# Kernel tuning notes

Hardware: AMD Instinct MI355X
Metric: run time of the kernel (lower is better)

Reference implementation:

```python
import jax, jax.numpy as jnp
import numpy as np

B, T, S, DM, H, HID = 4, 1024, 1024, 1024, 16, 4096
DEPTH = DM // H


def setup_inputs() -> dict:
    key = jax.random.key(0)
    ks = jax.random.split(key, 32)
    n = lambda k, shape, scale=1.0: jax.random.normal(k, shape, dtype=jnp.float32) * scale
    w_scale = 1.0 / np.sqrt(DM)
    inp = {
        "x": n(ks[0], (B, T, DM)),
        "enc_out": n(ks[1], (B, S, DM)),
        # causal mask: 1 where attention is forbidden (TF convention mask*-1e9)
        "look_ahead_mask": jnp.broadcast_to(
            jnp.triu(jnp.ones((T, T), jnp.float32), k=1), (B, 1, T, T)),
        "padding_mask": jnp.zeros((B, 1, 1, S), jnp.float32),
    }
    # self-attention MHA params
    names = ["wq1", "wk1", "wv1", "wo1", "wq2", "wk2", "wv2", "wo2"]
    for i, nm in enumerate(names):
        inp[nm] = n(ks[2 + i], (DM, DM), w_scale)
        inp["b" + nm[1:]] = jnp.zeros((DM,), jnp.float32)
    # FFN
    inp["wh"] = n(ks[10], (DM, HID), w_scale)
    inp["bh"] = jnp.zeros((HID,), jnp.float32)
    inp["wout"] = n(ks[11], (HID, DM), 1.0 / np.sqrt(HID))
    inp["bout"] = jnp.zeros((DM,), jnp.float32)
    for i in (1, 2, 3):
        inp[f"g{i}"] = jnp.ones((DM,), jnp.float32)
        inp[f"be{i}"] = jnp.zeros((DM,), jnp.float32)
    return inp


def _layer_norm(x, gamma, beta, eps=1e-6):
    mean = jnp.mean(x, axis=-1, keepdims=True)
    var = jnp.mean(jnp.square(x - mean), axis=-1, keepdims=True)
    return gamma * (x - mean) * jax.lax.rsqrt(var + eps) + beta


def _mha(q_in, k_in, v_in, mask, wq, bq, wk, bk, wv, bv, wo, bo):
    b = q_in.shape[0]
    split = lambda t: t.reshape(b, -1, H, DEPTH).transpose(0, 2, 1, 3)  # [b,h,s,d]
    Q = split(q_in @ wq + bq)
    K = split(k_in @ wk + bk)
    V = split(v_in @ wv + bv)
    scores = jnp.einsum("bhqd,bhkd->bhqk", Q, K) / jnp.sqrt(jnp.float32(DEPTH))
    scores = scores + mask * (-1e9)
    w = jax.nn.softmax(scores, axis=-1)
    out = jnp.einsum("bhqk,bhkd->bhqd", w, V)
    out = out.transpose(0, 2, 1, 3).reshape(b, -1, DM)
    return out @ wo + bo


def reference(x, enc_out, look_ahead_mask, padding_mask,
              wq1, bq1, wk1, bk1, wv1, bv1, wo1, bo1,
              wq2, bq2, wk2, bk2, wv2, bv2, wo2, bo2,
              wh, bh, wout, bout, g1, be1, g2, be2, g3, be3):
    # self-attention + residual + LN (dropout identity at inference)
    a1 = _mha(x, x, x, look_ahead_mask, wq1, bq1, wk1, bk1, wv1, bv1, wo1, bo1)
    h1 = _layer_norm(a1 + x, g1, be1)
    # cross-attention + residual + LN
    a2 = _mha(h1, enc_out, enc_out, padding_mask,
              wq2, bq2, wk2, bk2, wv2, bv2, wo2, bo2)
    h2 = _layer_norm(a2 + h1, g2, be2)
    # FFN + residual + LN
    f = jax.nn.relu(h2 @ wh + bh) @ wout + bout
    return _layer_norm(f + h2, g3, be3)
```

## Files before the change

kernel.cpp:

```cpp
#include <hip/hip_runtime.h>
#include <hip/hip_bf16.h>

typedef __bf16 bf16;
typedef __bf16 bf16x4 __attribute__((ext_vector_type(4)));
typedef __bf16 bf16x8 __attribute__((ext_vector_type(8)));
typedef float floatx4 __attribute__((ext_vector_type(4)));

#define MFMA16(a, b, c) __builtin_amdgcn_mfma_f32_16x16x32_bf16(a, b, c, 0, 0, 0)

#define BB   4
#define TT   1024
#define SS   1024
#define DMOD 1024
#define NH   16
#define DH   64
#define HID  4096
#define MTOT (BB * TT)

__device__ __forceinline__ float loadf(const bf16* p)  { return (float)*p; }
__device__ __forceinline__ float loadf(const float* p) { return *p; }

__device__ __forceinline__ void gll16(const bf16* g, bf16* l) {
    __builtin_amdgcn_global_load_lds(
        (const __attribute__((address_space(1))) void*)g,
        (__attribute__((address_space(3))) void*)l, 16, 0, 0);
}

struct TBatch { const float* src[8]; bf16* dst[8]; };

__global__ __launch_bounds__(256)
void transpose_sq_kernel(TBatch tb)
{
    __shared__ float t[64][65];
    const float* W = tb.src[blockIdx.z];
    bf16* WT = tb.dst[blockIdx.z];
    const int k0 = blockIdx.y * 64, n0 = blockIdx.x * 64;
    const int tid = threadIdx.x;
    const int r = tid >> 4, c = (tid & 15) * 4;
    #pragma unroll
    for (int i = 0; i < 4; ++i) {
        float4 v = *(const float4*)(W + (size_t)(k0 + i * 16 + r) * DMOD + n0 + c);
        t[i * 16 + r][c + 0] = v.x; t[i * 16 + r][c + 1] = v.y;
        t[i * 16 + r][c + 2] = v.z; t[i * 16 + r][c + 3] = v.w;
    }
    __syncthreads();
    #pragma unroll
    for (int i = 0; i < 4; ++i) {
        int n = i * 16 + r;
        bf16x4 o;
        #pragma unroll
        for (int j = 0; j < 4; ++j) o[j] = (bf16)t[c + j][n];
        *(bf16x4*)(WT + (size_t)(n0 + n) * DMOD + k0 + c) = o;
    }
}

__global__ __launch_bounds__(256)
void transpose_kernel(const float* __restrict__ W, bf16* __restrict__ WT, int K, int N)
{
    __shared__ float t[64][65];
    const int k0 = blockIdx.y * 64, n0 = blockIdx.x * 64;
    const int tid = threadIdx.x;
    const int r = tid >> 4, c = (tid & 15) * 4;
    #pragma unroll
    for (int i = 0; i < 4; ++i) {
        float4 v = *(const float4*)(W + (size_t)(k0 + i * 16 + r) * N + n0 + c);
        t[i * 16 + r][c + 0] = v.x; t[i * 16 + r][c + 1] = v.y;
        t[i * 16 + r][c + 2] = v.z; t[i * 16 + r][c + 3] = v.w;
    }
    __syncthreads();
    #pragma unroll
    for (int i = 0; i < 4; ++i) {
        int n = i * 16 + r;
        bf16x4 o;
        #pragma unroll
        for (int j = 0; j < 4; ++j) o[j] = (bf16)t[c + j][n];
        *(bf16x4*)(WT + (size_t)(n0 + n) * K + k0 + c) = o;
    }
}

__global__ __launch_bounds__(256)
void vtrans_kernel(const bf16* __restrict__ in, int ldi, bf16* __restrict__ out)
{
    __shared__ bf16 t[64][72];
    const int r0 = blockIdx.y * 64;
    const int c0 = blockIdx.x * 64;
    const int tid = threadIdx.x;
    const int rr = tid >> 3;
    const int c8 = (tid & 7) * 8;
    #pragma unroll
    for (int i = 0; i < 2; ++i) {
        int row = i * 32 + rr;
        bf16x8 v = *(const bf16x8*)(in + (size_t)(r0 + row) * ldi + c0 + c8);
        *(bf16x8*)(&t[row][c8]) = v;
    }
    __syncthreads();
    #pragma unroll
    for (int i = 0; i < 2; ++i) {
        int col = i * 32 + rr;
        bf16x8 v;
        #pragma unroll
        for (int j = 0; j < 8; ++j) v[j] = t[c8 + j][col];
        *(bf16x8*)(out + (size_t)(c0 + col) * MTOT + r0 + c8) = v;
    }
}

__global__ __launch_bounds__(256)
void cvt_kernel(const float* __restrict__ in, bf16* __restrict__ out, int n4)
{
    int i = blockIdx.x * 256 + threadIdx.x;
    if (i < n4) {
        float4 v = ((const float4*)in)[i];
        bf16x4 o = { (bf16)v.x, (bf16)v.y, (bf16)v.z, (bf16)v.w };
        ((bf16x4*)out)[i] = o;
    }
}

__global__ __launch_bounds__(256)
void bias_concat_kernel(const float* bq1, const float* bk1, const float* bv1,
                        const float* bk2, const float* bv2, float* __restrict__ biasc)
{
    int i = blockIdx.x * 256 + threadIdx.x;
    float v;
    if      (i < 1024) v = bq1[i];
    else if (i < 2048) v = bk1[i - 1024];
    else if (i < 3072) v = bv1[i - 2048];
    else if (i < 4096) v = bk2[i - 3072];
    else               v = bv2[i - 4096];
    if (i < 5120) biasc[i] = v;
}

template <int EPI, typename TR>
__global__ __launch_bounds__(256, 2)
void gemm_kernel(const bf16* __restrict__ A, int lda, const bf16* __restrict__ B,
                 const float* __restrict__ bias, const TR* __restrict__ resid,
                 bf16* __restrict__ out, int M, int N, int K)
{
    __shared__ bf16 Al[128 * 64];
    __shared__ bf16 Bl[128 * 64];

    const int tid  = threadIdx.x;
    const int wave = tid >> 6;
    const int lane = tid & 63;
    const int l16  = lane & 15;
    const int quad = lane >> 4;
    const int bm   = blockIdx.y * 128;
    const int bn   = blockIdx.x * 128;
    const int wm   = (wave >> 1) * 64;
    const int wn   = (wave & 1) * 64;
    const int lrow = lane >> 3;
    const int lcol = (lane & 7) * 8;

    floatx4 acc[4][4] = {};

    for (int k0 = 0; k0 < K; k0 += 64) {
        __syncthreads();
        #pragma unroll
        for (int t = 0; t < 4; ++t) {
            int r0 = (wave * 4 + t) * 8;
            gll16(A + (size_t)(bm + r0 + lrow) * lda + k0 + lcol, Al + r0 * 64);
            gll16(B + (size_t)(bn + r0 + lrow) * K   + k0 + lcol, Bl + r0 * 64);
        }
        __syncthreads();

        #pragma unroll
        for (int ks = 0; ks < 2; ++ks) {
            bf16x8 af[4], bg[4];
            #pragma unroll
            for (int mt = 0; mt < 4; ++mt)
                af[mt] = *(const bf16x8*)(Al + (wm + mt * 16 + l16) * 64 + ks * 32 + quad * 8);
            #pragma unroll
            for (int nt = 0; nt < 4; ++nt)
                bg[nt] = *(const bf16x8*)(Bl + (wn + nt * 16 + l16) * 64 + ks * 32 + quad * 8);
            #pragma unroll
            for (int mt = 0; mt < 4; ++mt)
                #pragma unroll
                for (int nt = 0; nt < 4; ++nt)
                    acc[mt][nt] = MFMA16(af[mt], bg[nt], acc[mt][nt]);
        }
    }

    #pragma unroll
    for (int mt = 0; mt < 4; ++mt) {
        int row0 = bm + wm + mt * 16 + quad * 4;
        #pragma unroll
        for (int nt = 0; nt < 4; ++nt) {
            int col = bn + wn + nt * 16 + l16;
            float bv = bias[col];
            #pragma unroll
            for (int r = 0; r < 4; ++r) {
                float v = acc[mt][nt][r] + bv;
                size_t idx = (size_t)(row0 + r) * N + col;
                if (EPI == 1) v = fmaxf(v, 0.0f);
                if (EPI == 2) v += loadf(resid + idx);
                out[idx] = (bf16)v;
            }
        }
    }
}

template <int EPI, typename TR>
__global__ __launch_bounds__(256, 2)
void gemm64_kernel(const bf16* __restrict__ A, int lda, const bf16* __restrict__ B,
                   const float* __restrict__ bias, const TR* __restrict__ resid,
                   bf16* __restrict__ out, int M, int N, int K)
{
    __shared__ bf16 Al[64 * 64];
    __shared__ bf16 Bl[128 * 64];

    const int tid  = threadIdx.x;
    const int wave = tid >> 6;
    const int lane = tid & 63;
    const int l16  = lane & 15;
    const int quad = lane >> 4;
    const int bm   = blockIdx.y * 64;
    const int bn   = blockIdx.x * 128;
    const int wm   = (wave >> 1) * 32;
    const int wn   = (wave & 1) * 64;
    const int lrow = lane >> 3;
    const int lcol = (lane & 7) * 8;

    floatx4 acc[2][4] = {};

    for (int k0 = 0; k0 < K; k0 += 64) {
        __syncthreads();
        #pragma unroll
        for (int t = 0; t < 2; ++t) {
            int r0 = wave * 16 + t * 8;
            gll16(A + (size_t)(bm + r0 + lrow) * lda + k0 + lcol, Al + r0 * 64);
        }
        #pragma unroll
        for (int t = 0; t < 4; ++t) {
            int r0 = (wave * 4 + t) * 8;
            gll16(B + (size_t)(bn + r0 + lrow) * K + k0 + lcol, Bl + r0 * 64);
        }
        __syncthreads();

        #pragma unroll
        for (int ks = 0; ks < 2; ++ks) {
            bf16x8 af[2], bg[4];
            #pragma unroll
            for (int mt = 0; mt < 2; ++mt)
                af[mt] = *(const bf16x8*)(Al + (wm + mt * 16 + l16) * 64 + ks * 32 + quad * 8);
            #pragma unroll
            for (int nt = 0; nt < 4; ++nt)
                bg[nt] = *(const bf16x8*)(Bl + (wn + nt * 16 + l16) * 64 + ks * 32 + quad * 8);
            #pragma unroll
            for (int mt = 0; mt < 2; ++mt)
                #pragma unroll
                for (int nt = 0; nt < 4; ++nt)
                    acc[mt][nt] = MFMA16(af[mt], bg[nt], acc[mt][nt]);
        }
    }

    #pragma unroll
    for (int mt = 0; mt < 2; ++mt) {
        int row0 = bm + wm + mt * 16 + quad * 4;
        #pragma unroll
        for (int nt = 0; nt < 4; ++nt) {
            int col = bn + wn + nt * 16 + l16;
            float bv = bias[col];
            #pragma unroll
            for (int r = 0; r < 4; ++r) {
                float v = acc[mt][nt][r] + bv;
                size_t idx = (size_t)(row0 + r) * N + col;
                if (EPI == 1) v = fmaxf(v, 0.0f);
                if (EPI == 2) v += loadf(resid + idx);
                out[idx] = (bf16)v;
            }
        }
    }
}

template <int CAUSAL>
__global__ __launch_bounds__(256, 2)
void attn_kernel(const bf16* __restrict__ Q, int ldq, const bf16* __restrict__ K, int ldk,
                 const bf16* __restrict__ Vt, bf16* __restrict__ O, int ldo)
{
    __shared__ bf16 Kl[64 * 64];
    __shared__ bf16 Vl[64 * 64];
    __shared__ bf16 Pl[4 * 16 * 72];

    const int tid  = threadIdx.x;
    const int wave = tid >> 6;
    const int lane = tid & 63;
    const int l16  = lane & 15;
    const int quad = lane >> 4;
    const int qb   = CAUSAL ? (15 - blockIdx.x) : blockIdx.x;
    const int h    = blockIdx.y;
    const int b    = blockIdx.z;

    const int qrow0 = b * TT + qb * 64 + wave * 16;
    const int colh  = h * DH;
    const int lr8   = lane >> 3;
    const int lc8   = (lane & 7) * 8;

    bf16x8 qa[2];
    #pragma unroll
    for (int c = 0; c < 2; ++c)
        qa[c] = *(const bf16x8*)(Q + (size_t)(qrow0 + l16) * ldq + colh + c * 32 + quad * 8);

    floatx4 o[5] = {};
    const float C = 0.125f * 1.4426950408889634f;
    bf16x8 onesf;
    {
        bf16 ov = (bf16)((l16 == 0) ? 1.0f : 0.0f);
        #pragma unroll
        for (int j = 0; j < 8; ++j) onesf[j] = ov;
    }

    const int ntiles = CAUSAL ? qb + 1 : (SS / 64);
    bf16* pw = Pl + wave * (16 * 72);

    for (int t = 0; t < ntiles; ++t) {
        const int kv0 = t * 64;
        __syncthreads();
        #pragma unroll
        for (int i = 0; i < 2; ++i) {
            int r0 = wave * 16 + i * 8;
            gll16(K  + (size_t)(b * SS + kv0 + r0 + lr8) * ldk + colh + lc8, Kl + r0 * 64);
            gll16(Vt + (size_t)(colh + r0 + lr8) * MTOT + b * SS + kv0 + lc8, Vl + r0 * 64);
        }
        __syncthreads();

        floatx4 s[4];
        #pragma unroll
        for (int nt = 0; nt < 4; ++nt) {
            bf16x8 kb0 = *(const bf16x8*)(Kl + (nt * 16 + l16) * 64 + quad * 8);
            bf16x8 kb1 = *(const bf16x8*)(Kl + (nt * 16 + l16) * 64 + 32 + quad * 8);
            floatx4 z = {};
            z = MFMA16(qa[0], kb0, z);
            z = MFMA16(qa[1], kb1, z);
            s[nt] = z;
        }

        const bool dm = CAUSAL && (t == qb);
        #pragma unroll
        for (int nt = 0; nt < 4; ++nt)
            #pragma unroll
            for (int r = 0; r < 4; ++r) {
                float sv = s[nt][r] * C;
                if (dm) {
                    int qg  = wave * 16 + quad * 4 + r;
                    int kvg = nt * 16 + l16;
                    if (kvg > qg) sv = -1e30f;
                }
                float pv = exp2f(sv);
                pw[(quad * 4 + r) * 72 + nt * 16 + l16] = (bf16)pv;
            }

        bf16x8 pa0 = *(const bf16x8*)(pw + l16 * 72 + quad * 8);
        bf16x8 pa1 = *(const bf16x8*)(pw + l16 * 72 + 32 + quad * 8);
        #pragma unroll
        for (int dt = 0; dt < 4; ++dt) {
            bf16x8 vb0 = *(const bf16x8*)(Vl + (dt * 16 + l16) * 64 + quad * 8);
            bf16x8 vb1 = *(const bf16x8*)(Vl + (dt * 16 + l16) * 64 + 32 + quad * 8);
            o[dt] = MFMA16(pa0, vb0, o[dt]);
            o[dt] = MFMA16(pa1, vb1, o[dt]);
        }
        o[4] = MFMA16(pa0, onesf, o[4]);
        o[4] = MFMA16(pa1, onesf, o[4]);
    }

    #pragma unroll
    for (int r = 0; r < 4; ++r) {
        float lr  = __shfl(o[4][r], (lane & 48));
        float inv = __builtin_amdgcn_rcpf(lr);
        #pragma unroll
        for (int dt = 0; dt < 4; ++dt) {
            float ov = o[dt][r] * inv;
            size_t idx = (size_t)(qrow0 + quad * 4 + r) * ldo + colh + dt * 16 + l16;
            O[idx] = (bf16)ov;
        }
    }
}

template <typename TO>
__global__ __launch_bounds__(256)
void ln_kernel(const bf16* __restrict__ in, const float* __restrict__ g,
               const float* __restrict__ be, TO* __restrict__ out)
{
    const int row = blockIdx.x;
    const int tid = threadIdx.x;
    bf16x4 xv = *(const bf16x4*)(in + (size_t)row * DMOD + tid * 4);
    float x0 = (float)xv[0], x1 = (float)xv[1], x2 = (float)xv[2], x3 = (float)xv[3];

    float s = x0 + x1 + x2 + x3;
    #pragma unroll
    for (int off = 32; off >= 1; off >>= 1) s += __shfl_xor(s, off);
    __shared__ float red1[4];
    __shared__ float red2[4];
    const int wave = tid >> 6;
    if ((tid & 63) == 0) red1[wave] = s;
    __syncthreads();
    float mean = (red1[0] + red1[1] + red1[2] + red1[3]) * (1.0f / DMOD);

    float d0 = x0 - mean, d1 = x1 - mean, d2 = x2 - mean, d3 = x3 - mean;
    float sq = d0 * d0 + d1 * d1 + d2 * d2 + d3 * d3;
    #pragma unroll
    for (int off = 32; off >= 1; off >>= 1) sq += __shfl_xor(sq, off);
    if ((tid & 63) == 0) red2[wave] = sq;
    __syncthreads();
    float var = (red2[0] + red2[1] + red2[2] + red2[3]) * (1.0f / DMOD);
    float rs = rsqrtf(var + 1e-6f);

    int c = tid * 4;
    size_t o0 = (size_t)row * DMOD + c;
    out[o0 + 0] = (TO)(g[c + 0] * d0 * rs + be[c + 0]);
    out[o0 + 1] = (TO)(g[c + 1] * d1 * rs + be[c + 1]);
    out[o0 + 2] = (TO)(g[c + 2] * d2 * rs + be[c + 2]);
    out[o0 + 3] = (TO)(g[c + 3] * d3 * rs + be[c + 3]);
}

extern "C" void kernel_launch(void* const* d_in, const int* in_sizes, int n_in,
                              void* d_out, int out_size, void* d_ws, size_t ws_size,
                              hipStream_t stream)
{
    const float* x   = (const float*)d_in[0];
    const float* enc = (const float*)d_in[1];
    const float* wq1 = (const float*)d_in[4];  const float* bq1 = (const float*)d_in[5];
    const float* wk1 = (const float*)d_in[6];  const float* bk1 = (const float*)d_in[7];
    const float* wv1 = (const float*)d_in[8];  const float* bv1 = (const float*)d_in[9];
    const float* wo1 = (const float*)d_in[10]; const float* bo1 = (const float*)d_in[11];
    const float* wq2 = (const float*)d_in[12]; const float* bq2 = (const float*)d_in[13];
    const float* wk2 = (const float*)d_in[14]; const float* bk2 = (const float*)d_in[15];
    const float* wv2 = (const float*)d_in[16]; const float* bv2 = (const float*)d_in[17];
    const float* wo2 = (const float*)d_in[18]; const float* bo2 = (const float*)d_in[19];
    const float* wh  = (const float*)d_in[20]; const float* bh  = (const float*)d_in[21];
    const float* wou = (const float*)d_in[22]; const float* bou = (const float*)d_in[23];
    const float* g1  = (const float*)d_in[24]; const float* be1 = (const float*)d_in[25];
    const float* g2  = (const float*)d_in[26]; const float* be2 = (const float*)d_in[27];
    const float* g3  = (const float*)d_in[28]; const float* be3 = (const float*)d_in[29];

    const int M = MTOT;
    const size_t MB = 1u << 20;
    dim3 blk(256);

    char* ws = (char*)d_ws;
    bf16*  WT    = (bf16*)(ws);
    float* biasc = (float*)(ws + 8 * MB);
    bf16*  xb    = (bf16*)(ws + 9 * MB);
    bf16*  h1    = (bf16*)(ws + 9 * MB);
    bf16*  tmpb3 = (bf16*)(ws + 9 * MB);
    bf16*  encb  = (bf16*)(ws + 17 * MB);
    bf16*  Vt2   = (bf16*)(ws + 17 * MB);
    bf16*  ffn   = (bf16*)(ws + 17 * MB);
    bf16*  qkv   = (bf16*)(ws + 25 * MB);
    bf16*  kvb   = qkv + (size_t)M * 1024;
    bf16*  tmpb2 = qkv + (size_t)M * 1024;
    bf16*  Vt1   = (bf16*)(ws + 49 * MB);
    bf16*  tmpb1 = (bf16*)(ws + 49 * MB);
    bf16*  h2    = (bf16*)(ws + 49 * MB);

    dim3 gThi(HID / 64, DMOD / 64);
    dim3 gTout(DMOD / 64, HID / 64);
    dim3 gVt(DMOD / 64, M / 64);
    dim3 gQKV(3072 / 128, M / 128);
    dim3 gKV(2048 / 128, M / 128);
    dim3 gN64(DMOD / 128, M / 64);
    dim3 gH(HID / 128, M / 128);
    dim3 gA(TT / 64, NH, BB);
    const size_t W1M = (size_t)1024 * 1024;

    cvt_kernel<<<dim3(M * DMOD / 4 / 256), blk, 0, stream>>>(x, xb, M * DMOD / 4);
    cvt_kernel<<<dim3(M * DMOD / 4 / 256), blk, 0, stream>>>(enc, encb, M * DMOD / 4);
    bias_concat_kernel<<<dim3(20), blk, 0, stream>>>(bq1, bk1, bv1, bk2, bv2, biasc);

    {
        TBatch tb;
        tb.src[0] = wq1; tb.dst[0] = WT + 0 * W1M;
        tb.src[1] = wk1; tb.dst[1] = WT + 1 * W1M;
        tb.src[2] = wv1; tb.dst[2] = WT + 2 * W1M;
        tb.src[3] = wo1; tb.dst[3] = WT + 3 * W1M;
        tb.src[4] = tb.src[5] = tb.src[6] = tb.src[7] = wq1;
        tb.dst[4] = tb.dst[5] = tb.dst[6] = tb.dst[7] = WT;
        dim3 g4(16, 16, 4);
        transpose_sq_kernel<<<g4, blk, 0, stream>>>(tb);
    }

    gemm_kernel<0, bf16><<<gQKV, blk, 0, stream>>>(xb, 1024, WT, biasc, (const bf16*)nullptr,
                                                   qkv, M, 3072, 1024);
    vtrans_kernel<<<gVt, blk, 0, stream>>>(qkv + 2048, 3072, Vt1);
    attn_kernel<1><<<gA, blk, 0, stream>>>(qkv, 3072, qkv + 1024, 3072, Vt1, qkv, 3072);
    gemm64_kernel<2, float><<<gN64, blk, 0, stream>>>(qkv, 3072, WT + 3 * W1M, bo1, x,
                                                      tmpb1, M, 1024, 1024);
    ln_kernel<bf16><<<dim3(M), blk, 0, stream>>>(tmpb1, g1, be1, h1);

    {
        TBatch tb;
        tb.src[0] = wq2; tb.dst[0] = WT + 0 * W1M;
        tb.src[1] = wk2; tb.dst[1] = WT + 1 * W1M;
        tb.src[2] = wv2; tb.dst[2] = WT + 2 * W1M;
        tb.src[3] = wo2; tb.dst[3] = WT + 3 * W1M;
        tb.src[4] = tb.src[5] = tb.src[6] = tb.src[7] = wq2;
        tb.dst[4] = tb.dst[5] = tb.dst[6] = tb.dst[7] = WT;
        dim3 g4(16, 16, 4);
        transpose_sq_kernel<<<g4, blk, 0, stream>>>(tb);
    }

    gemm64_kernel<0, bf16><<<gN64, blk, 0, stream>>>(h1, 1024, WT, bq2, (const bf16*)nullptr,
                                                     qkv, M, 1024, 1024);
    gemm_kernel<0, bf16><<<gKV, blk, 0, stream>>>(encb, 1024, WT + 1 * W1M, biasc + 3072,
                                                  (const bf16*)nullptr, kvb, M, 2048, 1024);
    vtrans_kernel<<<gVt, blk, 0, stream>>>(kvb + 1024, 2048, Vt2);
    attn_kernel<0><<<gA, blk, 0, stream>>>(qkv, 1024, kvb, 2048, Vt2, qkv, 1024);
    gemm64_kernel<2, bf16><<<gN64, blk, 0, stream>>>(qkv, 1024, WT + 3 * W1M, bo2, h1,
                                                     tmpb2, M, 1024, 1024);
    ln_kernel<bf16><<<dim3(M), blk, 0, stream>>>(tmpb2, g2, be2, h2);

    transpose_kernel<<<gThi, blk, 0, stream>>>(wh, WT, DMOD, HID);
    gemm_kernel<1, bf16><<<gH, blk, 0, stream>>>(h2, 1024, WT, bh, (const bf16*)nullptr,
                                                 ffn, M, HID, 1024);
    transpose_kernel<<<gTout, blk, 0, stream>>>(wou, WT, HID, DMOD);
    gemm64_kernel<2, bf16><<<gN64, blk, 0, stream>>>(ffn, 4096, WT, bou, h2,
                                                     tmpb3, M, 1024, 4096);
    ln_kernel<float><<<dim3(M), blk, 0, stream>>>(tmpb3, g3, be3, (float*)d_out);
}
```

Baseline: 573.4 us.

## Double-buffer LDS tiles with prefetch and XOR-swizzle in GEMM and attention

Converts the GEMM, GEMM64 and attention kernels to double-buffered LDS: each loop iteration issues global-to-LDS loads for the next K or KV tile before running MFMAs on the current one, and uses a single barrier per iteration instead of two. It also XOR-swizzles the 16-byte column chunks within each 64-element row, both when staging and when reading fragments, to reduce LDS bank conflicts. LDS use doubles (64KB for the 128x128 GEMM), which may limit the two-blocks-per-CU occupancy target.

Measured after the change: 543.6 us. 1.05x faster.

```diff
diff --git a/kernel.cpp b/kernel.cpp
--- a/kernel.cpp
+++ b/kernel.cpp
@@ -135,8 +135,8 @@
                  const float* __restrict__ bias, const TR* __restrict__ resid,
                  bf16* __restrict__ out, int M, int N, int K)
 {
-    __shared__ bf16 Al[128 * 64];
-    __shared__ bf16 Bl[128 * 64];
+    __shared__ bf16 Al[2][128 * 64];
+    __shared__ bf16 Bl[2][128 * 64];
 
     const int tid  = threadIdx.x;
     const int wave = tid >> 6;
@@ -148,36 +148,53 @@
     const int wm   = (wave >> 1) * 64;
     const int wn   = (wave & 1) * 64;
     const int lrow = lane >> 3;
-    const int lcol = (lane & 7) * 8;
+    const int scol = ((lane & 7) ^ lrow) * 8;
 
     floatx4 acc[4][4] = {};
-
-    for (int k0 = 0; k0 < K; k0 += 64) {
-        __syncthreads();
-        #pragma unroll
-        for (int t = 0; t < 4; ++t) {
-            int r0 = (wave * 4 + t) * 8;
-            gll16(A + (size_t)(bm + r0 + lrow) * lda + k0 + lcol, Al + r0 * 64);
-            gll16(B + (size_t)(bn + r0 + lrow) * K   + k0 + lcol, Bl + r0 * 64);
-        }
-        __syncthreads();
-
+    const int ntk = K / 64;
+
+    auto STAGE = [&](int kt, int buf) {
+        const int k0 = kt * 64;
+        #pragma unroll
+        for (int i = 0; i < 4; ++i) {
+            int r0 = (wave * 4 + i) * 8;
+            gll16(A + (size_t)(bm + r0 + lrow) * lda + k0 + scol, &Al[buf][r0 * 64]);
+            gll16(B + (size_t)(bn + r0 + lrow) * K   + k0 + scol, &Bl[buf][r0 * 64]);
+        }
+    };
+
+    auto COMPUTE = [&](int buf) {
         #pragma unroll
         for (int ks = 0; ks < 2; ++ks) {
             bf16x8 af[4], bg[4];
+            const int xo = ((ks * 4 + quad) ^ (l16 & 7)) * 8;
             #pragma unroll
             for (int mt = 0; mt < 4; ++mt)
-                af[mt] = *(const bf16x8*)(Al + (wm + mt * 16 + l16) * 64 + ks * 32 + quad * 8);
+                af[mt] = *(const bf16x8*)(&Al[buf][(wm + mt * 16 + l16) * 64 + xo]);
             #pragma unroll
             for (int nt = 0; nt < 4; ++nt)
-                bg[nt] = *(const bf16x8*)(Bl + (wn + nt * 16 + l16) * 64 + ks * 32 + quad * 8);
+                bg[nt] = *(const bf16x8*)(&Bl[buf][(wn + nt * 16 + l16) * 64 + xo]);
             #pragma unroll
             for (int mt = 0; mt < 4; ++mt)
                 #pragma unroll
                 for (int nt = 0; nt < 4; ++nt)
                     acc[mt][nt] = MFMA16(af[mt], bg[nt], acc[mt][nt]);
         }
-    }
+    };
+
+    STAGE(0, 0);
+    asm volatile("s_waitcnt vmcnt(0)" ::: "memory");
+    __builtin_amdgcn_s_barrier();
+
+    int cur = 0;
+    for (int t = 0; t < ntk - 1; ++t) {
+        STAGE(t + 1, cur ^ 1);
+        COMPUTE(cur);
+        asm volatile("s_waitcnt vmcnt(0) lgkmcnt(0)" ::: "memory");
+        __builtin_amdgcn_s_barrier();
+        cur ^= 1;
+    }
+    COMPUTE(cur);
 
     #pragma unroll
     for (int mt = 0; mt < 4; ++mt) {
@@ -204,8 +221,8 @@
                    const float* __restrict__ bias, const TR* __restrict__ resid,
                    bf16* __restrict__ out, int M, int N, int K)
 {
-    __shared__ bf16 Al[64 * 64];
-    __shared__ bf16 Bl[128 * 64];
+    __shared__ bf16 Al[2][64 * 64];
+    __shared__ bf16 Bl[2][128 * 64];
 
     const int tid  = threadIdx.x;
     const int wave = tid >> 6;
@@ -217,40 +234,57 @@
     const int wm   = (wave >> 1) * 32;
     const int wn   = (wave & 1) * 64;
     const int lrow = lane >> 3;
-    const int lcol = (lane & 7) * 8;
+    const int scol = ((lane & 7) ^ lrow) * 8;
 
     floatx4 acc[2][4] = {};
-
-    for (int k0 = 0; k0 < K; k0 += 64) {
-        __syncthreads();
-        #pragma unroll
-        for (int t = 0; t < 2; ++t) {
-            int r0 = wave * 16 + t * 8;
-            gll16(A + (size_t)(bm + r0 + lrow) * lda + k0 + lcol, Al + r0 * 64);
-        }
-        #pragma unroll
-        for (int t = 0; t < 4; ++t) {
-            int r0 = (wave * 4 + t) * 8;
-            gll16(B + (size_t)(bn + r0 + lrow) * K + k0 + lcol, Bl + r0 * 64);
-        }
-        __syncthreads();
-
+    const int ntk = K / 64;
+
+    auto STAGE = [&](int kt, int buf) {
+        const int k0 = kt * 64;
+        #pragma unroll
+        for (int i = 0; i < 2; ++i) {
+            int r0 = wave * 16 + i * 8;
+            gll16(A + (size_t)(bm + r0 + lrow) * lda + k0 + scol, &Al[buf][r0 * 64]);
+        }
+        #pragma unroll
+        for (int i = 0; i < 4; ++i) {
+            int r0 = (wave * 4 + i) * 8;
+            gll16(B + (size_t)(bn + r0 + lrow) * K + k0 + scol, &Bl[buf][r0 * 64]);
+        }
+    };
+
+    auto COMPUTE = [&](int buf) {
         #pragma unroll
         for (int ks = 0; ks < 2; ++ks) {
             bf16x8 af[2], bg[4];
+            const int xo = ((ks * 4 + quad) ^ (l16 & 7)) * 8;
             #pragma unroll
             for (int mt = 0; mt < 2; ++mt)
-                af[mt] = *(const bf16x8*)(Al + (wm + mt * 16 + l16) * 64 + ks * 32 + quad * 8);
+                af[mt] = *(const bf16x8*)(&Al[buf][(wm + mt * 16 + l16) * 64 + xo]);
             #pragma unroll
             for (int nt = 0; nt < 4; ++nt)
-                bg[nt] = *(const bf16x8*)(Bl + (wn + nt * 16 + l16) * 64 + ks * 32 + quad * 8);
+                bg[nt] = *(const bf16x8*)(&Bl[buf][(wn + nt * 16 + l16) * 64 + xo]);
             #pragma unroll
             for (int mt = 0; mt < 2; ++mt)
                 #pragma unroll
                 for (int nt = 0; nt < 4; ++nt)
                     acc[mt][nt] = MFMA16(af[mt], bg[nt], acc[mt][nt]);
         }
-    }
+    };
+
+    STAGE(0, 0);
+    asm volatile("s_waitcnt vmcnt(0)" ::: "memory");
+    __builtin_amdgcn_s_barrier();
+
+    int cur = 0;
+    for (int t = 0; t < ntk - 1; ++t) {
+        STAGE(t + 1, cur ^ 1);
+        COMPUTE(cur);
+        asm volatile("s_waitcnt vmcnt(0) lgkmcnt(0)" ::: "memory");
+        __builtin_amdgcn_s_barrier();
+        cur ^= 1;
+    }
+    COMPUTE(cur);
 
     #pragma unroll
     for (int mt = 0; mt < 2; ++mt) {
@@ -276,8 +310,8 @@
 void attn_kernel(const bf16* __restrict__ Q, int ldq, const bf16* __restrict__ K, int ldk,
                  const bf16* __restrict__ Vt, bf16* __restrict__ O, int ldo)
 {
-    __shared__ bf16 Kl[64 * 64];
-    __shared__ bf16 Vl[64 * 64];
+    __shared__ bf16 Kl[2][64 * 64];
+    __shared__ bf16 Vl[2][64 * 64];
     __shared__ bf16 Pl[4 * 16 * 72];
 
     const int tid  = threadIdx.x;
@@ -292,7 +326,7 @@
     const int qrow0 = b * TT + qb * 64 + wave * 16;
     const int colh  = h * DH;
     const int lr8   = lane >> 3;
-    const int lc8   = (lane & 7) * 8;
+    const int lc8s  = ((lane & 7) ^ lr8) * 8;
 
     bf16x8 qa[2];
     #pragma unroll
@@ -311,22 +345,25 @@
     const int ntiles = CAUSAL ? qb + 1 : (SS / 64);
     bf16* pw = Pl + wave * (16 * 72);
 
-    for (int t = 0; t < ntiles; ++t) {
+    auto STAGE = [&](int t, int buf) {
         const int kv0 = t * 64;
-        __syncthreads();
         #pragma unroll
         for (int i = 0; i < 2; ++i) {
             int r0 = wave * 16 + i * 8;
-            gll16(K  + (size_t)(b * SS + kv0 + r0 + lr8) * ldk + colh + lc8, Kl + r0 * 64);
-            gll16(Vt + (size_t)(colh + r0 + lr8) * MTOT + b * SS + kv0 + lc8, Vl + r0 * 64);
-        }
-        __syncthreads();
+            gll16(K  + (size_t)(b * SS + kv0 + r0 + lr8) * ldk + colh + lc8s, &Kl[buf][r0 * 64]);
+            gll16(Vt + (size_t)(colh + r0 + lr8) * MTOT + b * SS + kv0 + lc8s, &Vl[buf][r0 * 64]);
+        }
+    };
+
+    auto COMPUTE = [&](int t, int buf) {
+        const int xo0 = (quad ^ (l16 & 7)) * 8;
+        const int xo1 = ((4 + quad) ^ (l16 & 7)) * 8;
 
         floatx4 s[4];
         #pragma unroll
         for (int nt = 0; nt < 4; ++nt) {
-            bf16x8 kb0 = *(const bf16x8*)(Kl + (nt * 16 + l16) * 64 + quad * 8);
-            bf16x8 kb1 = *(const bf16x8*)(Kl + (nt * 16 + l16) * 64 + 32 + quad * 8);
+            bf16x8 kb0 = *(const bf16x8*)(&Kl[buf][(nt * 16 + l16) * 64 + xo0]);
+            bf16x8 kb1 = *(const bf16x8*)(&Kl[buf][(nt * 16 + l16) * 64 + xo1]);
             floatx4 z = {};
             z = MFMA16(qa[0], kb0, z);
             z = MFMA16(qa[1], kb1, z);
@@ -352,14 +389,28 @@
         bf16x8 pa1 = *(const bf16x8*)(pw + l16 * 72 + 32 + quad * 8);
         #pragma unroll
         for (int dt = 0; dt < 4; ++dt) {
-            bf16x8 vb0 = *(const bf16x8*)(Vl + (dt * 16 + l16) * 64 + quad * 8);
-            bf16x8 vb1 = *(const bf16x8*)(Vl + (dt * 16 + l16) * 64 + 32 + quad * 8);
+            bf16x8 vb0 = *(const bf16x8*)(&Vl[buf][(dt * 16 + l16) * 64 + xo0]);
+            bf16x8 vb1 = *(const bf16x8*)(&Vl[buf][(dt * 16 + l16) * 64 + xo1]);
             o[dt] = MFMA16(pa0, vb0, o[dt]);
             o[dt] = MFMA16(pa1, vb1, o[dt]);
         }
         o[4] = MFMA16(pa0, onesf, o[4]);
         o[4] = MFMA16(pa1, onesf, o[4]);
-    }
+    };
+
+    STAGE(0, 0);
+    asm volatile("s_waitcnt vmcnt(0)" ::: "memory");
+    __builtin_amdgcn_s_barrier();
+
+    int cur = 0;
+    for (int t = 0; t < ntiles - 1; ++t) {
+        STAGE(t + 1, cur ^ 1);
+        COMPUTE(t, cur);
+        asm volatile("s_waitcnt vmcnt(0) lgkmcnt(0)" ::: "memory");
+        __builtin_amdgcn_s_barrier();
+        cur ^= 1;
+    }
+    COMPUTE(ntiles - 1, cur);
 
     #pragma unroll
     for (int r = 0; r < 4; ++r) {
```
